# Performance work log

Hardware: AMD Instinct MI355X
Metric: run time of the kernel (lower is better)

The kernel has to match this reference:

```python
import jax, jax.numpy as jnp
import numpy as np

B, N, E, H = 4, 2048, 1024, 16
D = E // H  # head dim = 64


def setup_inputs() -> dict:
    key = jax.random.key(0)
    k1, k2, k3 = jax.random.split(key, 3)
    x = jax.random.normal(k1, (B, N, E), dtype=jnp.float32)
    # torch nn.Linear weights are [out_features, in_features]
    w_qkv = jax.random.normal(k2, (3 * E, E), dtype=jnp.float32) * (E ** -0.5)
    w_out = jax.random.normal(k3, (E, E), dtype=jnp.float32) * (E ** -0.5)
    return {"x": x, "w_qkv": w_qkv, "w_out": w_out}


def reference(x, w_qkv, w_out):
    # fused QKV projection: [B,N,E] @ [E,3E] -> [B,N,3E]
    qkv = jnp.einsum("bne,fe->bnf", x, w_qkv)
    q, k, v = jnp.split(qkv, 3, axis=-1)
    # b n (h d) -> b h n d
    split_heads = lambda t: t.reshape(B, N, H, D).transpose(0, 2, 1, 3)
    q, k, v = map(split_heads, (q, k, v))
    scale = D ** -0.5
    scores = jnp.einsum("bhnd,bhmd->bhnm", q, k) * scale
    attn = jax.nn.softmax(scores, axis=-1)
    out = jnp.einsum("bhnm,bhmd->bhnd", attn, v)
    # b h n d -> b n (h d)
    out = out.transpose(0, 2, 1, 3).reshape(B, N, E)
    return jnp.einsum("bne,fe->bnf", out, w_out)
```

## Files before the change

kernel.cpp:

```cpp
#include <hip/hip_runtime.h>
#include <hip/hip_bf16.h>

typedef short bf16x8 __attribute__((ext_vector_type(8)));
typedef float f32x4 __attribute__((ext_vector_type(4)));
using bf16 = __hip_bfloat16;

#define MFMA16(a, b, c) __builtin_amdgcn_mfma_f32_16x16x32_bf16(a, b, c, 0, 0, 0)

typedef unsigned int u32;
typedef u32 __attribute__((address_space(1))) global_u32;
typedef u32 __attribute__((address_space(3))) lds_u32;

__device__ __forceinline__ void gload_lds16(const unsigned short* g, unsigned short* l) {
    __builtin_amdgcn_global_load_lds((const global_u32*)g, (lds_u32*)l, 16, 0, 0);
}

__device__ __forceinline__ short f2b(float f) {
    __hip_bfloat16 h = __float2bfloat16(f);
    return *reinterpret_cast<short*>(&h);
}

__device__ __forceinline__ float exp2_fast(float x) {
    float r;
    asm("v_exp_f32 %0, %1" : "=v"(r) : "v"(x));
    return r;
}

#define QSCALE 0.18033688011112042f

__global__ __launch_bounds__(256) void cvt3_kernel(const float* __restrict__ x,
                                                   const float* __restrict__ wq,
                                                   const float* __restrict__ wo,
                                                   unsigned short* __restrict__ xb,
                                                   unsigned short* __restrict__ wqb,
                                                   unsigned short* __restrict__ wob) {
    const int id = blockIdx.x;
    const float* src;
    unsigned short* dst;
    size_t off;
    if (id < 4096) {
        src = x; dst = xb; off = (size_t)id * 2048;
    } else if (id < 5632) {
        src = wq; dst = wqb; off = (size_t)(id - 4096) * 2048;
    } else {
        src = wo; dst = wob; off = (size_t)(id - 5632) * 2048;
    }
    const size_t i = off + (size_t)threadIdx.x * 8;
    float4 v0 = *(const float4*)(src + i);
    float4 v1 = *(const float4*)(src + i + 4);
    bf16x8 o;
    o[0] = f2b(v0.x); o[1] = f2b(v0.y); o[2] = f2b(v0.z); o[3] = f2b(v0.w);
    o[4] = f2b(v1.x); o[5] = f2b(v1.y); o[6] = f2b(v1.z); o[7] = f2b(v1.w);
    *(bf16x8*)(dst + i) = o;
}

template <int MODE, int NTN>
__global__ __launch_bounds__(512, 2) void gemm256x128_kernel(
    const unsigned short* __restrict__ A,
    const unsigned short* __restrict__ W,
    void* __restrict__ outp) {
    __shared__ unsigned short As[2][256][64];
    __shared__ unsigned short Bs[2][128][64];
    const int tid = threadIdx.x;
    const int lane = tid & 63;
    const int w = tid >> 6;
    const int wr = w >> 1, wc = w & 1;
    const int lm = lane & 15, quad = lane >> 4;

    constexpr int TPX = 4 * NTN;
    const int id = blockIdx.x;
    const int xs = (id & 7) * TPX + (id >> 3);
    const int n0 = (xs % NTN) * 128;
    const int m0 = (xs / NTN) * 256;

    const int sr = lane >> 3;
    const int sg = (lane & 7) ^ sr;
    const unsigned short* Ab = A + (size_t)(m0 + w * 8 + sr) * 1024 + sg * 8;
    const unsigned short* Wb = W + (size_t)(n0 + w * 8 + sr) * 1024 + sg * 8;

    f32x4 acc[4][4] = {};
    bf16x8 af[2][2];
    bf16x8 bfA[2][2];
    bf16x8 bfB[2][2];

#define STAGE_A(buf, half, kk)                                                     \
    do {                                                                           \
        gload_lds16(Ab + (size_t)((half) * 128) * 1024 + (kk),                     \
                    &As[buf][(half) * 128 + w * 8][0]);                            \
        gload_lds16(Ab + (size_t)((half) * 128 + 64) * 1024 + (kk),                \
                    &As[buf][(half) * 128 + 64 + w * 8][0]);                       \
    } while (0)
#define STAGE_B(buf, kk)                                                           \
    do {                                                                           \
        gload_lds16(Wb + (kk), &Bs[buf][w * 8][0]);                                \
        gload_lds16(Wb + (size_t)64 * 1024 + (kk), &Bs[buf][64 + w * 8][0]);       \
    } while (0)
#define LDA(buf, mh)                                                               \
    do {                                                                           \
        _Pragma("unroll") for (int mt2 = 0; mt2 < 2; mt2++)                        \
            _Pragma("unroll") for (int ks = 0; ks < 2; ks++)                       \
                af[mt2][ks] =                                                      \
                    *(const bf16x8*)&As[buf][wr * 64 + ((mh) * 2 + mt2) * 16 + lm] \
                                        [(((quad + ks * 4) ^ (lm & 7)) * 8)];      \
    } while (0)
#define LDB(buf, nh, DST)                                                          \
    do {                                                                           \
        _Pragma("unroll") for (int nt2 = 0; nt2 < 2; nt2++)                        \
            _Pragma("unroll") for (int ks = 0; ks < 2; ks++)                       \
                DST[nt2][ks] =                                                     \
                    *(const bf16x8*)&Bs[buf][wc * 64 + ((nh) * 2 + nt2) * 16 + lm] \
                                        [(((quad + ks * 4) ^ (lm & 7)) * 8)];      \
    } while (0)
#define PHASE_MM(mh, nh, BF)                                                       \
    do {                                                                           \
        __builtin_amdgcn_s_barrier();                                              \
        asm volatile("s_waitcnt lgkmcnt(0)" ::: "memory");                         \
        __builtin_amdgcn_s_setprio(1);                                             \
        _Pragma("unroll") for (int mt2 = 0; mt2 < 2; mt2++)                        \
            _Pragma("unroll") for (int nt2 = 0; nt2 < 2; nt2++) {                  \
                f32x4 t0 = MFMA16(af[mt2][0], BF[nt2][0],                          \
                                  acc[(mh) * 2 + mt2][(nh) * 2 + nt2]);            \
                acc[(mh) * 2 + mt2][(nh) * 2 + nt2] =                              \
                    MFMA16(af[mt2][1], BF[nt2][1], t0);                            \
            }                                                                      \
        __builtin_amdgcn_s_setprio(0);                                             \
        __builtin_amdgcn_s_barrier();                                              \
    } while (0)
#define VMCNT2 asm volatile("s_waitcnt vmcnt(2)" ::: "memory")

    STAGE_A(0, 0, 0); STAGE_A(0, 1, 0);
    STAGE_B(0, 0);
    STAGE_B(1, 64);
    VMCNT2;
    __builtin_amdgcn_s_barrier();

    for (int i = 0; i < 8; i++) {
        const int t = 2 * i;
        const int k1 = (t + 1) * 64;
        const int k2 = (t + 2 < 16) ? (t + 2) * 64 : 0;
        const int k3 = (t + 3 < 16) ? (t + 3) * 64 : 0;
        LDA(0, 0); LDB(0, 0, bfA);
        STAGE_A(1, 0, k1);
        PHASE_MM(0, 0, bfA);
        LDB(0, 1, bfB);
        STAGE_A(1, 1, k1);
        PHASE_MM(0, 1, bfB);
        LDA(0, 1);
        STAGE_B(0, k2);
        PHASE_MM(1, 1, bfB);
        VMCNT2;
        PHASE_MM(1, 0, bfA);
        LDA(1, 0); LDB(1, 0, bfA);
        STAGE_A(0, 0, k2);
        PHASE_MM(0, 0, bfA);
        LDB(1, 1, bfB);
        STAGE_A(0, 1, k2);
        PHASE_MM(0, 1, bfB);
        LDA(1, 1);
        STAGE_B(1, k3);
        PHASE_MM(1, 1, bfB);
        VMCNT2;
        PHASE_MM(1, 0, bfA);
    }

    asm volatile("s_waitcnt vmcnt(0)" ::: "memory");

    if (MODE == 2) {
        bf16* qkv = (bf16*)outp;
#pragma unroll
        for (int mt = 0; mt < 4; mt++)
#pragma unroll
            for (int nt = 0; nt < 4; nt++) {
                f32x4 v = acc[mt][nt];
                const int gr0 = m0 + wr * 64 + mt * 16 + quad * 4;
                const int gc = n0 + wc * 64 + nt * 16 + lm;
                const int which = gc >> 10;
                const int h = (gc >> 6) & 15;
                const int d = gc & 63;
                const int b = gr0 >> 11, n = gr0 & 2047;
                if (which == 2) {
                    short4 pk;
                    pk.x = f2b(v[0]); pk.y = f2b(v[1]); pk.z = f2b(v[2]); pk.w = f2b(v[3]);
                    *(short4*)&qkv[2ull * 8388608 +
                                   ((size_t)((b * 16 + h) * 64 + d)) * 2048 + n] = pk;
                } else {
#pragma unroll
                    for (int r = 0; r < 4; r++) {
                        float val = v[r];
                        if (which == 0) val *= QSCALE;
                        qkv[(size_t)which * 8388608 +
                            ((size_t)((b * 16 + h) * 2048 + n + r)) * 64 + d] =
                            __float2bfloat16(val);
                    }
                }
            }
    } else {
        float* o = (float*)outp;
#pragma unroll
        for (int mt = 0; mt < 4; mt++)
#pragma unroll
            for (int nt = 0; nt < 4; nt++) {
                f32x4 v = acc[mt][nt];
                const int gr0 = m0 + wr * 64 + mt * 16 + quad * 4;
                const int gc = n0 + wc * 64 + nt * 16 + lm;
#pragma unroll
                for (int r = 0; r < 4; r++) o[(size_t)(gr0 + r) * 1024 + gc] = v[r];
            }
    }
#undef STAGE_A
#undef STAGE_B
#undef LDA
#undef LDB
#undef PHASE_MM
#undef VMCNT2
}

__global__ __launch_bounds__(256, 2) void attn_mfma_kernel(
    const unsigned short* __restrict__ Qg, const unsigned short* __restrict__ Kg,
    const unsigned short* __restrict__ Vtg, unsigned short* __restrict__ O) {
    __shared__ unsigned short Ks[2][64][64];
    __shared__ unsigned short Vs[2][64][64];
    __shared__ unsigned short Ps[4][4][16][64];
    const int tid = threadIdx.x;
    const int lane = tid & 63;
    const int w = tid >> 6;
    const int lm = lane & 15;
    const int quad = lane >> 4;
    const int bh = blockIdx.x & 63;
    const int n0 = (blockIdx.x >> 6) * 256;
    const size_t base = (size_t)bh * (2048 * 64);

    bf16x8 qf[4][2];
#pragma unroll
    for (int mt = 0; mt < 4; mt++)
#pragma unroll
        for (int ks = 0; ks < 2; ks++)
            qf[mt][ks] = *(const bf16x8*)&Qg[base +
                                            (size_t)(n0 + w * 64 + mt * 16 + lm) * 64 +
                                            ks * 32 + quad * 8];

    f32x4 accO[4][4] = {};
    float lst[4] = {0.f, 0.f, 0.f, 0.f};

    const int sr = lane >> 3;
    const int sg = (lane & 7) ^ sr;

#pragma unroll
    for (int j = 0; j < 2; j++) {
        const int row = w * 16 + j * 8 + sr;
        gload_lds16(&Vtg[base + (size_t)row * 2048 + sg * 8], &Vs[0][w * 16 + j * 8][0]);
        gload_lds16(&Kg[base + (size_t)row * 64 + sg * 8], &Ks[0][w * 16 + j * 8][0]);
    }

    int kb = 0;
    for (int t = 0; t < 32; t++) {
        asm volatile("s_waitcnt vmcnt(0)" ::: "memory");
        __builtin_amdgcn_s_barrier();

        if (t + 1 < 32) {
            const int k0n = (t + 1) * 64;
#pragma unroll
            for (int j = 0; j < 2; j++) {
                const int row = w * 16 + j * 8 + sr;
                gload_lds16(&Vtg[base + (size_t)row * 2048 + k0n + sg * 8],
                            &Vs[kb ^ 1][w * 16 + j * 8][0]);
                gload_lds16(&Kg[base + (size_t)(k0n + row) * 64 + sg * 8],
                            &Ks[kb ^ 1][w * 16 + j * 8][0]);
            }
        }

        bf16x8 kbf[4][2];
#pragma unroll
        for (int kt = 0; kt < 4; kt++)
#pragma unroll
            for (int ks = 0; ks < 2; ks++)
                kbf[kt][ks] = *(const bf16x8*)&Ks[kb][kt * 16 + lm]
                                                 [(((ks * 4 + quad) ^ (lm & 7)) * 8)];

#pragma unroll
        for (int mt = 0; mt < 4; mt++) {
            f32x4 s[4];
            __builtin_amdgcn_s_setprio(1);
#pragma unroll
            for (int kt = 0; kt < 4; kt++) {
                f32x4 z = {};
                z = MFMA16(kbf[kt][0], qf[mt][0], z);
                s[kt] = MFMA16(kbf[kt][1], qf[mt][1], z);
            }
            __builtin_amdgcn_s_setprio(0);
            float ps = 0.f;
#pragma unroll
            for (int kt = 0; kt < 4; kt++) {
                const float p0 = exp2_fast(s[kt][0]);
                const float p1 = exp2_fast(s[kt][1]);
                const float p2 = exp2_fast(s[kt][2]);
                const float p3 = exp2_fast(s[kt][3]);
                ps += (p0 + p1) + (p2 + p3);
                short4 pk;
                pk.x = f2b(p0); pk.y = f2b(p1); pk.z = f2b(p2); pk.w = f2b(p3);
                const int g = kt * 2 + (quad >> 1);
                *(short4*)&Ps[w][mt][lm][((g ^ (lm & 7)) * 8) + (quad & 1) * 4] = pk;
            }
            lst[mt] += ps;
        }

        bf16x8 vbf[4][2];
#pragma unroll
        for (int nt = 0; nt < 4; nt++)
#pragma unroll
            for (int ks = 0; ks < 2; ks++)
                vbf[nt][ks] = *(const bf16x8*)&Vs[kb][nt * 16 + lm]
                                                 [(((ks * 4 + quad) ^ (lm & 7)) * 8)];
#pragma unroll
        for (int mt = 0; mt < 4; mt++) {
            bf16x8 pb0 = *(const bf16x8*)&Ps[w][mt][lm][(((quad) ^ (lm & 7)) * 8)];
            bf16x8 pb1 = *(const bf16x8*)&Ps[w][mt][lm][(((4 + quad) ^ (lm & 7)) * 8)];
            __builtin_amdgcn_s_setprio(1);
#pragma unroll
            for (int nt = 0; nt < 4; nt++) {
                f32x4 a = MFMA16(vbf[nt][0], pb0, accO[mt][nt]);
                accO[mt][nt] = MFMA16(vbf[nt][1], pb1, a);
            }
            __builtin_amdgcn_s_setprio(0);
        }

        kb ^= 1;
    }

#pragma unroll
    for (int mt = 0; mt < 4; mt++) {
        lst[mt] += __shfl_xor(lst[mt], 16);
        lst[mt] += __shfl_xor(lst[mt], 32);
    }

    const int b = bh >> 4, h = bh & 15;
#pragma unroll
    for (int mt = 0; mt < 4; mt++) {
        const float inv = 1.0f / lst[mt];
        const int n = n0 + w * 64 + mt * 16 + lm;
#pragma unroll
        for (int nt = 0; nt < 4; nt++) {
            short4 pk;
            pk.x = f2b(accO[mt][nt][0] * inv);
            pk.y = f2b(accO[mt][nt][1] * inv);
            pk.z = f2b(accO[mt][nt][2] * inv);
            pk.w = f2b(accO[mt][nt][3] * inv);
            *(short4*)&O[((size_t)(b * 2048 + n)) * 1024 + h * 64 + nt * 16 + quad * 4] = pk;
        }
    }
}

extern "C" void kernel_launch(void* const* d_in, const int* in_sizes, int n_in,
                              void* d_out, int out_size, void* d_ws, size_t ws_size,
                              hipStream_t stream) {
    const float* x = (const float*)d_in[0];
    const float* w_qkv = (const float*)d_in[1];
    const float* w_out = (const float*)d_in[2];
    float* out = (float*)d_out;

    unsigned short* qkvb = (unsigned short*)d_ws;
    unsigned short* xb = qkvb + 3ull * 8388608;
    unsigned short* wqkvb = xb + 8388608;
    unsigned short* woutb = wqkvb + 3145728;

    cvt3_kernel<<<6144, 256, 0, stream>>>(x, w_qkv, w_out, xb, wqkvb, woutb);
    gemm256x128_kernel<2, 24><<<768, 512, 0, stream>>>(xb, wqkvb, (void*)qkvb);
    attn_mfma_kernel<<<512, 256, 0, stream>>>(qkvb, qkvb + 8388608,
                                              qkvb + 2 * 8388608, xb);
    gemm256x128_kernel<1, 8><<<256, 512, 0, stream>>>(xb, woutb, (void*)out);
}
```

Baseline: 251.4 us.

## Collapse GEMM k-step from four quarter phases into two half phases

```diff
diff --git a/kernel.cpp b/kernel.cpp
--- a/kernel.cpp
+++ b/kernel.cpp
@@ -79,7 +79,7 @@
     const unsigned short* Wb = W + (size_t)(n0 + w * 8 + sr) * 1024 + sg * 8;
 
     f32x4 acc[4][4] = {};
-    bf16x8 af[2][2];
+    bf16x8 af[4][2];
     bf16x8 bfA[2][2];
     bf16x8 bfB[2][2];
 
@@ -95,12 +95,12 @@
         gload_lds16(Wb + (kk), &Bs[buf][w * 8][0]);                                \
         gload_lds16(Wb + (size_t)64 * 1024 + (kk), &Bs[buf][64 + w * 8][0]);       \
     } while (0)
-#define LDA(buf, mh)                                                               \
-    do {                                                                           \
-        _Pragma("unroll") for (int mt2 = 0; mt2 < 2; mt2++)                        \
+#define LDA_FULL(buf)                                                              \
+    do {                                                                           \
+        _Pragma("unroll") for (int mt2 = 0; mt2 < 4; mt2++)                        \
             _Pragma("unroll") for (int ks = 0; ks < 2; ks++)                       \
                 af[mt2][ks] =                                                      \
-                    *(const bf16x8*)&As[buf][wr * 64 + ((mh) * 2 + mt2) * 16 + lm] \
+                    *(const bf16x8*)&As[buf][wr * 64 + mt2 * 16 + lm]              \
                                         [(((quad + ks * 4) ^ (lm & 7)) * 8)];      \
     } while (0)
 #define LDB(buf, nh, DST)                                                          \
@@ -111,16 +111,16 @@
                     *(const bf16x8*)&Bs[buf][wc * 64 + ((nh) * 2 + nt2) * 16 + lm] \
                                         [(((quad + ks * 4) ^ (lm & 7)) * 8)];      \
     } while (0)
-#define PHASE_MM(mh, nh, BF)                                                       \
+#define PHASE_MM2(nh, BF)                                                          \
     do {                                                                           \
         __builtin_amdgcn_s_barrier();                                              \
         asm volatile("s_waitcnt lgkmcnt(0)" ::: "memory");                         \
         __builtin_amdgcn_s_setprio(1);                                             \
-        _Pragma("unroll") for (int mt2 = 0; mt2 < 2; mt2++)                        \
+        _Pragma("unroll") for (int mt2 = 0; mt2 < 4; mt2++)                        \
             _Pragma("unroll") for (int nt2 = 0; nt2 < 2; nt2++) {                  \
                 f32x4 t0 = MFMA16(af[mt2][0], BF[nt2][0],                          \
-                                  acc[(mh) * 2 + mt2][(nh) * 2 + nt2]);            \
-                acc[(mh) * 2 + mt2][(nh) * 2 + nt2] =                              \
+                                  acc[mt2][(nh) * 2 + nt2]);                       \
+                acc[mt2][(nh) * 2 + nt2] =                                         \
                     MFMA16(af[mt2][1], BF[nt2][1], t0);                            \
             }                                                                      \
         __builtin_amdgcn_s_setprio(0);                                             \
@@ -139,28 +139,20 @@
         const int k1 = (t + 1) * 64;
         const int k2 = (t + 2 < 16) ? (t + 2) * 64 : 0;
         const int k3 = (t + 3 < 16) ? (t + 3) * 64 : 0;
-        LDA(0, 0); LDB(0, 0, bfA);
-        STAGE_A(1, 0, k1);
-        PHASE_MM(0, 0, bfA);
-        LDB(0, 1, bfB);
-        STAGE_A(1, 1, k1);
-        PHASE_MM(0, 1, bfB);
-        LDA(0, 1);
+        LDA_FULL(0);
+        LDB(0, 0, bfA); LDB(0, 1, bfB);
+        STAGE_A(1, 0, k1); STAGE_A(1, 1, k1);
+        PHASE_MM2(0, bfA);
         STAGE_B(0, k2);
-        PHASE_MM(1, 1, bfB);
         VMCNT2;
-        PHASE_MM(1, 0, bfA);
-        LDA(1, 0); LDB(1, 0, bfA);
-        STAGE_A(0, 0, k2);
-        PHASE_MM(0, 0, bfA);
-        LDB(1, 1, bfB);
-        STAGE_A(0, 1, k2);
-        PHASE_MM(0, 1, bfB);
-        LDA(1, 1);
+        PHASE_MM2(1, bfB);
+        LDA_FULL(1);
+        LDB(1, 0, bfA); LDB(1, 1, bfB);
+        STAGE_A(0, 0, k2); STAGE_A(0, 1, k2);
+        PHASE_MM2(0, bfA);
         STAGE_B(1, k3);
-        PHASE_MM(1, 1, bfB);
         VMCNT2;
-        PHASE_MM(1, 0, bfA);
+        PHASE_MM2(1, bfB);
     }
 
     asm volatile("s_waitcnt vmcnt(0)" ::: "memory");
@@ -209,9 +201,9 @@
     }
 #undef STAGE_A
 #undef STAGE_B
-#undef LDA
+#undef LDA_FULL
 #undef LDB
-#undef PHASE_MM
+#undef PHASE_MM2
 #undef VMCNT2
 }
 
```

Result: faster. 242.7 us (-3.4%).
